# Kernel tuning notes

Hardware: AMD Instinct MI355X
Metric: run time of the kernel (lower is better)

The kernel has to match this reference:

```python
import jax, jax.numpy as jnp
import numpy as np

B, T, IN = 4096, 64, 3
D, H, NB = 128, 4, 2
DH = D // H  # 32
EPS = 1e-5


def layer_norm(x, g, b):
    mu = x.mean(-1, keepdims=True)
    v = x.var(-1, keepdims=True)
    return (x - mu) / jnp.sqrt(v + EPS) * g + b


def group_norm(x, g, b):
    # headwise GroupNorm over the last dim split into H groups of DH
    xr = x.reshape(x.shape[:-1] + (H, DH))
    mu = xr.mean(-1, keepdims=True)
    v = xr.var(-1, keepdims=True)
    xn = ((xr - mu) / jnp.sqrt(v + EPS)).reshape(x.shape)
    return xn * g + b


def slstm(xg, R):
    # xg: [B,T,4,D] input-driven gate preactivations (i,f,z,o)
    # R : [4,H,DH,DH] block-diagonal (per-head) recurrent kernels per gate
    Bb = xg.shape[0]

    def step(carry, g):
        h, c, n, m = carry  # each [B,D]
        r = jnp.einsum('bhd,ghde->bghe', h.reshape(Bb, H, DH), R).reshape(Bb, 4, D)
        g = g + r
        it, ft, zt, ot = g[:, 0], g[:, 1], g[:, 2], g[:, 3]
        m_new = jnp.maximum(ft + m, it)          # stabilizer state
        i = jnp.exp(it - m_new)                  # stabilized exp input gate
        f = jnp.exp(ft + m - m_new)              # stabilized exp forget gate
        c_new = f * c + i * jnp.tanh(zt)
        n_new = f * n + i                        # normalizer state
        h_new = jax.nn.sigmoid(ot) * c_new / n_new
        return (h_new, c_new, n_new, m_new), h_new

    init = tuple(jnp.zeros((Bb, D), xg.dtype) for _ in range(4))
    _, hs = jax.lax.scan(step, init, jnp.swapaxes(xg, 0, 1))  # [T,B,D]
    return jnp.swapaxes(hs, 0, 1)


def setup_inputs() -> dict:
    key = jax.random.key(0)
    ks = jax.random.split(key, 12)
    s_in = 1.0 / np.sqrt(IN)
    s_d = 1.0 / np.sqrt(D)
    inp = {
        'x': jax.random.normal(ks[0], (B, T, IN), jnp.float32),
        'w_in': jax.random.normal(ks[1], (IN, D), jnp.float32) * s_in,
        'b_in': jnp.zeros((D,), jnp.float32),
        'ln1_g': jnp.ones((NB, D), jnp.float32),
        'ln1_b': jnp.zeros((NB, D), jnp.float32),
        'Wg': jax.random.normal(ks[2], (NB, D, 4 * D), jnp.float32) * s_d,
        'bg': jnp.zeros((NB, 4 * D), jnp.float32),
        'Rg': jax.random.normal(ks[3], (NB, 4, H, DH, DH), jnp.float32) / np.sqrt(DH),
        'gn_g': jnp.ones((NB, D), jnp.float32),
        'gn_b': jnp.zeros((NB, D), jnp.float32),
        'ln2_g': jnp.ones((NB, D), jnp.float32),
        'ln2_b': jnp.zeros((NB, D), jnp.float32),
        'W1': jax.random.normal(ks[4], (NB, D, D), jnp.float32) * s_d,
        'W2': jax.random.normal(ks[5], (NB, D, D), jnp.float32) * s_d,
        'lnf_g': jnp.ones((D,), jnp.float32),
        'lnf_b': jnp.zeros((D,), jnp.float32),
        'w_out': jax.random.normal(ks[6], (D, 1), jnp.float32) * s_d,
        'b_out': jnp.zeros((1,), jnp.float32),
    }
    return inp


def reference(x, w_in, b_in, ln1_g, ln1_b, Wg, bg, Rg, gn_g, gn_b,
              ln2_g, ln2_b, W1, W2, lnf_g, lnf_b, w_out, b_out):
    h = x @ w_in + b_in  # [B,T,D]
    for blk in range(NB):
        # sLSTM sub-block (pre-LN residual)
        xn = layer_norm(h, ln1_g[blk], ln1_b[blk])
        xg = (xn @ Wg[blk] + bg[blk]).reshape(h.shape[0], T, 4, D)
        hs = slstm(xg, Rg[blk])
        h = h + group_norm(hs, gn_g[blk], gn_b[blk])
        # FFN sub-block (pre-LN residual, proj_factor=1.0, gelu, no bias)
        yn = layer_norm(h, ln2_g[blk], ln2_b[blk])
        h = h + jax.nn.gelu(yn @ W1[blk]) @ W2[blk]
    h = layer_norm(h, lnf_g, lnf_b)  # post-blocks norm
    out = (h[:, -1, :] @ w_out + b_out)[:, 0]  # [B]
    return out
```

## Files before the change

### kernel.cpp

```cpp
#include <hip/hip_runtime.h>
#include <hip/hip_bf16.h>
#include <cstdint>
#include <cstddef>

#define EPS 1e-5f
#define BB 4096
#define TT 64
#define NBLK 2
#define MROWS (BB * TT)

typedef unsigned short ushort_t;
typedef __attribute__((ext_vector_type(8))) short short8;
typedef __attribute__((ext_vector_type(4))) float floatx4;

__device__ __forceinline__ ushort_t f2b(float f) {
    __hip_bfloat16 h = __float2bfloat16(f);
    return *reinterpret_cast<ushort_t*>(&h);
}
__device__ __forceinline__ float tanh_fast(float z) {
    return 1.f - 2.f / (__expf(2.f * z) + 1.f);
}
__device__ __forceinline__ void lds_barrier() {
    asm volatile("s_waitcnt lgkmcnt(0)\n\ts_barrier" ::: "memory");
}

template <int CTRL>
__device__ __forceinline__ float ror_add(float v) {
    int r = __builtin_amdgcn_update_dpp(
        0, __builtin_bit_cast(int, v), CTRL, 0xf, 0xf, false);
    return v + __builtin_bit_cast(float, r);
}
__device__ __forceinline__ float red16(float v) {
    v = ror_add<0x121>(v);
    v = ror_add<0x122>(v);
    v = ror_add<0x124>(v);
    v = ror_add<0x128>(v);
    return v;
}

__global__ __launch_bounds__(256) void k_cvtall(
    const float* __restrict__ Wg, const float* __restrict__ W1,
    const float* __restrict__ W2, ushort_t* __restrict__ Wgt,
    ushort_t* __restrict__ W1t, ushort_t* __restrict__ W2t) {
    int idx = blockIdx.x * 256 + threadIdx.x;
    if (idx < 2 * 512 * 128) {
        int blk = idx >> 16, r = idx & 65535;
        int n = r >> 7, k = r & 127;
        Wgt[idx] = f2b(Wg[(size_t)blk * 65536 + k * 512 + n]);
    } else if (idx < 2 * 512 * 128 + 2 * 128 * 128) {
        int i2 = idx - 2 * 512 * 128;
        int blk = i2 >> 14, r = i2 & 16383;
        int n = r >> 7, k = r & 127;
        W1t[i2] = f2b(W1[(size_t)blk * 16384 + k * 128 + n]);
    } else {
        int i2 = idx - (2 * 512 * 128 + 2 * 128 * 128);
        int blk = i2 >> 14, r = i2 & 16383;
        int n = r >> 7, k = r & 127;
        W2t[i2] = f2b(W2[(size_t)blk * 16384 + k * 128 + n]);
    }
}

template <bool EMBED, bool LASTONLY>
__global__ __launch_bounds__(512, 2) void k_gslstm(
    float* __restrict__ h, const float* __restrict__ x,
    const float* __restrict__ w_in, const float* __restrict__ b_in,
    const ushort_t* __restrict__ Wgt, const float* __restrict__ bg,
    const float* __restrict__ Rg,
    const float* __restrict__ ln1g, const float* __restrict__ ln1b,
    const float* __restrict__ gng, const float* __restrict__ gnb) {
    __shared__ float xg_ring[2][512][20];
    __shared__ float hin_ring[3][16][132];
    __shared__ ushort_t Afrag[2][16][136];
    __shared__ ushort_t tpose[4][16][40];

    const int tid = threadIdx.x;
    const int lane = tid & 63;
    const int wave = tid >> 6;
    const int q = lane >> 4;
    const int ml = lane & 15;
    const int b0 = blockIdx.x * 16;

    if (wave < 4) {
        const int p = wave;
        const int row = p * 4 + q;
        short8 WB[4][8];
#pragma unroll
        for (int ks = 0; ks < 4; ++ks)
#pragma unroll
            for (int s = 0; s < 8; ++s)
                WB[ks][s] = *(const short8*)(Wgt +
                    ((size_t)(p * 128 + s * 16 + ml) * 128 + ks * 32 + q * 8));
        float biasv[8];
#pragma unroll
        for (int s = 0; s < 8; ++s) biasv[s] = bg[p * 128 + s * 16 + ml];

        auto issue_in = [&](int tt, float4& A, float4& B) {
            const float4* hp =
                (const float4*)(h + ((size_t)(b0 + row) * TT + tt) * 128 + ml * 8);
            A = hp[0]; B = hp[1];
        };
        auto issue_x = [&](int tt, float& x0, float& x1, float& x2) {
            const float* xp = x + ((size_t)(b0 + row) * TT + tt) * 3;
            x0 = xp[0]; x1 = xp[1]; x2 = xp[2];
        };
        auto embed_v = [&](float x0, float x1, float x2, float* v) {
            float4 w00 = *(const float4*)(w_in + 0 * 128 + ml * 8);
            float4 w01 = *(const float4*)(w_in + 0 * 128 + ml * 8 + 4);
            float4 w10 = *(const float4*)(w_in + 1 * 128 + ml * 8);
            float4 w11 = *(const float4*)(w_in + 1 * 128 + ml * 8 + 4);
            float4 w20 = *(const float4*)(w_in + 2 * 128 + ml * 8);
            float4 w21 = *(const float4*)(w_in + 2 * 128 + ml * 8 + 4);
            float4 be0 = *(const float4*)(b_in + ml * 8);
            float4 be1 = *(const float4*)(b_in + ml * 8 + 4);
            const float w0[8] = {w00.x, w00.y, w00.z, w00.w, w01.x, w01.y, w01.z, w01.w};
            const float w1[8] = {w10.x, w10.y, w10.z, w10.w, w11.x, w11.y, w11.z, w11.w};
            const float w2[8] = {w20.x, w20.y, w20.z, w20.w, w21.x, w21.y, w21.z, w21.w};
            const float be[8] = {be0.x, be0.y, be0.z, be0.w, be1.x, be1.y, be1.z, be1.w};
#pragma unroll
            for (int j = 0; j < 8; ++j)
                v[j] = x0 * w0[j] + x1 * w1[j] + x2 * w2[j] + be[j];
        };
        auto ln_stage = [&](const float* v, int aslot, int rslot) {
            float s = 0.f, ss = 0.f;
#pragma unroll
            for (int j = 0; j < 8; ++j) { s += v[j]; ss += v[j] * v[j]; }
            s = red16(s);
            ss = red16(ss);
            float mu = s * (1.f / 128.f);
            float rstd = rsqrtf(ss * (1.f / 128.f) - mu * mu + EPS);
            float4 g0 = *(const float4*)(ln1g + ml * 8);
            float4 g1 = *(const float4*)(ln1g + ml * 8 + 4);
            float4 c0 = *(const float4*)(ln1b + ml * 8);
            float4 c1 = *(const float4*)(ln1b + ml * 8 + 4);
            const float gg[8] = {g0.x, g0.y, g0.z, g0.w, g1.x, g1.y, g1.z, g1.w};
            const float bbv[8] = {c0.x, c0.y, c0.z, c0.w, c1.x, c1.y, c1.z, c1.w};
            ushort_t pk[8];
#pragma unroll
            for (int j = 0; j < 8; ++j)
                pk[j] = f2b((v[j] - mu) * rstd * gg[j] + bbv[j]);
            *(short8*)&Afrag[aslot][row][ml * 8] = *(const short8*)pk;
            *(float4*)&hin_ring[rslot][row][ml * 8] = *(const float4*)v;
            *(float4*)&hin_ring[rslot][row][ml * 8 + 4] = *(const float4*)(v + 4);
        };
        auto gemm_stage = [&](int slot) {
            short8 af[4];
#pragma unroll
            for (int ks = 0; ks < 4; ++ks)
                af[ks] = *(const short8*)&Afrag[slot][ml][ks * 32 + q * 8];
            floatx4 acc[8];
#pragma unroll
            for (int s = 0; s < 8; ++s) {
                float b = biasv[s];
                acc[s] = (floatx4){b, b, b, b};
            }
#pragma unroll
            for (int ks = 0; ks < 4; ++ks)
#pragma unroll
                for (int s = 0; s < 8; ++s)
                    acc[s] = __builtin_amdgcn_mfma_f32_16x16x32_bf16(
                        af[ks], WB[ks][s], acc[s], 0, 0, 0);
#pragma unroll
            for (int s = 0; s < 8; ++s)
                *(floatx4*)&xg_ring[slot][p * 128 + s * 16 + ml][q * 4] = acc[s];
        };

        float4 pA0, pA1, pB0, pB1;
        float px0 = 0.f, px1 = 0.f, px2 = 0.f, qx0 = 0.f, qx1 = 0.f, qx2 = 0.f;

        {
            float v[8];
            if (EMBED) {
                float a0, a1, a2, d0, d1, d2v;
                issue_x(0, a0, a1, a2);
                issue_x(1, d0, d1, d2v);
                issue_x(2, px0, px1, px2);
                embed_v(a0, a1, a2, v);  ln_stage(v, 0, 0);
                embed_v(d0, d1, d2v, v); ln_stage(v, 1, 1);
            } else {
                float4 a0, a1, d0, d1;
                issue_in(0, a0, a1);
                issue_in(1, d0, d1);
                issue_in(2, pA0, pA1);
                *(float4*)v = a0; *(float4*)(v + 4) = a1; ln_stage(v, 0, 0);
                *(float4*)v = d0; *(float4*)(v + 4) = d1; ln_stage(v, 1, 1);
            }
        }
        lds_barrier();
        gemm_stage(0);
        lds_barrier();

        int rs2 = 2, rs3 = 0;
#pragma unroll 1
        for (int t = 0; t < TT; t += 2) {
            if (t + 3 < TT) {
                if (EMBED) issue_x(t + 3, qx0, qx1, qx2);
                else       issue_in(t + 3, pB0, pB1);
            }
            gemm_stage((t + 1) & 1);
            if (t + 2 < TT) {
                float v[8];
                if (EMBED) embed_v(px0, px1, px2, v);
                else { *(float4*)v = pA0; *(float4*)(v + 4) = pA1; }
                ln_stage(v, t & 1, rs2);
            }
            lds_barrier();
            if (t + 4 < TT) {
                if (EMBED) issue_x(t + 4, px0, px1, px2);
                else       issue_in(t + 4, pA0, pA1);
            }
            if (t + 2 < TT) gemm_stage(t & 1);
            if (t + 3 < TT) {
                float v[8];
                if (EMBED) embed_v(qx0, qx1, qx2, v);
                else { *(float4*)v = pB0; *(float4*)(v + 4) = pB1; }
                ln_stage(v, (t + 1) & 1, rs3);
            }
            lds_barrier();
            rs2 += 2; if (rs2 >= 3) rs2 -= 3;
            rs3 += 2; if (rs3 >= 3) rs3 -= 3;
        }
    } else {
        __builtin_amdgcn_s_setprio(1);
        const int hd = wave - 4;
        short8 RB[4][2];
#pragma unroll
        for (int g = 0; g < 4; ++g)
#pragma unroll
            for (int d2 = 0; d2 < 2; ++d2) {
                ushort_t tmp[8];
#pragma unroll
                for (int j = 0; j < 8; ++j)
                    tmp[j] = f2b(Rg[(size_t)g * 4096 + hd * 1024 +
                                    (q * 8 + j) * 32 + d2 * 16 + ml]);
                RB[g][d2] = *(const short8*)tmp;
            }
        const float gng0 = gng[hd * 32 + ml], gng1 = gng[hd * 32 + 16 + ml];
        const float gnb0 = gnb[hd * 32 + ml], gnb1 = gnb[hd * 32 + 16 + ml];
        float cst[8], nst[8], mst[8];
#pragma unroll
        for (int i = 0; i < 8; ++i) { cst[i] = 0.f; nst[i] = 0.f; mst[i] = 0.f; }
        short8 h8 = {0, 0, 0, 0, 0, 0, 0, 0};

        auto scan_iter = [&](int t, int rs) {
            floatx4 acc[4][2];
#pragma unroll
            for (int g = 0; g < 4; ++g)
#pragma unroll
                for (int d2 = 0; d2 < 2; ++d2)
                    acc[g][d2] = *(const floatx4*)
                        &xg_ring[t & 1][g * 128 + hd * 32 + d2 * 16 + ml][q * 4];
#pragma unroll
            for (int g = 0; g < 4; ++g)
#pragma unroll
                for (int d2 = 0; d2 < 2; ++d2)
                    acc[g][d2] = __builtin_amdgcn_mfma_f32_16x16x32_bf16(
                        h8, RB[g][d2], acc[g][d2], 0, 0, 0);
            float hv[2][4];
#pragma unroll
            for (int d2 = 0; d2 < 2; ++d2)
#pragma unroll
                for (int r = 0; r < 4; ++r) {
                    const int si = d2 * 4 + r;
                    float it = acc[0][d2][r], ft = acc[1][d2][r];
                    float zt = acc[2][d2][r], ot = acc[3][d2][r];
                    float mn = fmaxf(ft + mst[si], it);
                    float iv = __expf(it - mn);
                    float fv = __expf(ft + mst[si] - mn);
                    float cn = fv * cst[si] + iv * tanh_fast(zt);
                    float nn = fv * nst[si] + iv;
                    hv[d2][r] = cn / (nn * (1.f + __expf(-ot)));
                    cst[si] = cn; nst[si] = nn; mst[si] = mn;
                }
#pragma unroll
            for (int d2 = 0; d2 < 2; ++d2)
#pragma unroll
                for (int r = 0; r < 4; ++r)
                    tpose[hd][q * 4 + r][d2 * 16 + ml] = f2b(hv[d2][r]);
            asm volatile("s_waitcnt lgkmcnt(0)" ::: "memory");
            h8 = *(const short8*)&tpose[hd][ml][q * 8];
            if (!LASTONLY || t == TT - 1) {
                float s[4], ss[4];
#pragma unroll
                for (int r = 0; r < 4; ++r) {
                    s[r] = hv[0][r] + hv[1][r];
                    ss[r] = hv[0][r] * hv[0][r] + hv[1][r] * hv[1][r];
                }
#pragma unroll
                for (int r = 0; r < 4; ++r) {
                    s[r] = red16(s[r]);
                    ss[r] = red16(ss[r]);
                }
#pragma unroll
                for (int r = 0; r < 4; ++r) {
                    float mu = s[r] * (1.f / 32.f);
                    float rstd = rsqrtf(ss[r] * (1.f / 32.f) - mu * mu + EPS);
#pragma unroll
                    for (int d2 = 0; d2 < 2; ++d2) {
                        float hin = hin_ring[rs][q * 4 + r][hd * 32 + d2 * 16 + ml];
                        float gv = d2 ? gng1 : gng0;
                        float bv = d2 ? gnb1 : gnb0;
                        h[((size_t)(b0 + q * 4 + r) * TT + t) * 128 +
                          hd * 32 + d2 * 16 + ml] =
                            hin + (hv[d2][r] - mu) * rstd * gv + bv;
                    }
                }
            }
        };

        lds_barrier();
        lds_barrier();
        int rs = 0;
#pragma unroll 1
        for (int t = 0; t < TT; t += 2) {
            scan_iter(t, rs);
            lds_barrier();
            scan_iter(t + 1, rs == 2 ? 0 : rs + 1);
            lds_barrier();
            rs += 2; if (rs >= 3) rs -= 3;
        }
    }
}

template <bool LAST>
__global__ __launch_bounds__(256, 6) void k_ffn(
    float* __restrict__ h, const ushort_t* __restrict__ W1t,
    const ushort_t* __restrict__ W2t,
    const float* __restrict__ lng, const float* __restrict__ lnb) {
    __shared__ ushort_t As[32][136];
    __shared__ ushort_t T1[32][136];
    int tid = threadIdx.x;
    int lane = tid & 63, wave = tid >> 6;
    int q = lane >> 4, ml = lane & 15;
    int wn = wave * 32;
    size_t row0 = (size_t)blockIdx.x * 32;

    short8 W1B[2][4];
#pragma unroll
    for (int jn = 0; jn < 2; ++jn)
#pragma unroll
        for (int ks = 0; ks < 4; ++ks)
            W1B[jn][ks] = *(const short8*)(W1t +
                ((size_t)(wn + jn * 16 + ml) * 128 + ks * 32 + q * 8));

    int r = tid >> 3, qd = tid & 7;
    size_t grow = LAST ? ((row0 + r) * TT + (TT - 1)) : (row0 + r);
    const float* hrow = h + grow * 128 + qd * 16;
    float s = 0.f, ss = 0.f;
#pragma unroll
    for (int k = 0; k < 4; ++k) {
        float4 v = ((const float4*)hrow)[k];
        s += v.x + v.y + v.z + v.w;
        ss += v.x * v.x + v.y * v.y + v.z * v.z + v.w * v.w;
    }
    s += __shfl_xor(s, 1); ss += __shfl_xor(ss, 1);
    s += __shfl_xor(s, 2); ss += __shfl_xor(ss, 2);
    s += __shfl_xor(s, 4); ss += __shfl_xor(ss, 4);
    float mu = s * (1.f / 128.f);
    float rstd = rsqrtf(ss * (1.f / 128.f) - mu * mu + EPS);
#pragma unroll
    for (int kk = 0; kk < 2; ++kk) {
        float4 a = ((const float4*)hrow)[2 * kk];
        float4 b = ((const float4*)hrow)[2 * kk + 1];
        int c0 = qd * 16 + kk * 8;
        float4 g0 = *(const float4*)(lng + c0);
        float4 g1 = *(const float4*)(lng + c0 + 4);
        float4 b0 = *(const float4*)(lnb + c0);
        float4 b1 = *(const float4*)(lnb + c0 + 4);
        ushort_t p[8];
        p[0] = f2b((a.x - mu) * rstd * g0.x + b0.x);
        p[1] = f2b((a.y - mu) * rstd * g0.y + b0.y);
        p[2] = f2b((a.z - mu) * rstd * g0.z + b0.z);
        p[3] = f2b((a.w - mu) * rstd * g0.w + b0.w);
        p[4] = f2b((b.x - mu) * rstd * g1.x + b1.x);
        p[5] = f2b((b.y - mu) * rstd * g1.y + b1.y);
        p[6] = f2b((b.z - mu) * rstd * g1.z + b1.z);
        p[7] = f2b((b.w - mu) * rstd * g1.w + b1.w);
        *(short8*)&As[r][c0] = *(const short8*)p;
    }
    lds_barrier();

    floatx4 acc[2][2];
#pragma unroll
    for (int i = 0; i < 2; ++i)
#pragma unroll
        for (int j = 0; j < 2; ++j) acc[i][j] = (floatx4)0.f;
#pragma unroll
    for (int ks = 0; ks < 4; ++ks) {
        short8 af[2];
#pragma unroll
        for (int im = 0; im < 2; ++im)
            af[im] = *(const short8*)&As[im * 16 + ml][ks * 32 + q * 8];
#pragma unroll
        for (int im = 0; im < 2; ++im)
#pragma unroll
            for (int jn = 0; jn < 2; ++jn)
                acc[im][jn] = __builtin_amdgcn_mfma_f32_16x16x32_bf16(
                    af[im], W1B[jn][ks], acc[im][jn], 0, 0, 0);
    }
#pragma unroll
    for (int im = 0; im < 2; ++im)
#pragma unroll
        for (int jn = 0; jn < 2; ++jn)
#pragma unroll
            for (int rr = 0; rr < 4; ++rr) {
                float v = acc[im][jn][rr];
                float u = 0.7978845608028654f * (v + 0.044715f * v * v * v);
                float gv = 0.5f * v * (1.f + tanh_fast(u));
                T1[im * 16 + q * 4 + rr][wn + jn * 16 + ml] = f2b(gv);
            }
    short8 W2B[2][4];
#pragma unroll
    for (int jn = 0; jn < 2; ++jn)
#pragma unroll
        for (int ks = 0; ks < 4; ++ks)
            W2B[jn][ks] = *(const short8*)(W2t +
                ((size_t)(wn + jn * 16 + ml) * 128 + ks * 32 + q * 8));
    lds_barrier();

#pragma unroll
    for (int i = 0; i < 2; ++i)
#pragma unroll
        for (int j = 0; j < 2; ++j) acc[i][j] = (floatx4)0.f;
#pragma unroll
    for (int ks = 0; ks < 4; ++ks) {
        short8 af[2];
#pragma unroll
        for (int im = 0; im < 2; ++im)
            af[im] = *(const short8*)&T1[im * 16 + ml][ks * 32 + q * 8];
#pragma unroll
        for (int im = 0; im < 2; ++im)
#pragma unroll
            for (int jn = 0; jn < 2; ++jn)
                acc[im][jn] = __builtin_amdgcn_mfma_f32_16x16x32_bf16(
                    af[im], W2B[jn][ks], acc[im][jn], 0, 0, 0);
    }
#pragma unroll
    for (int im = 0; im < 2; ++im)
#pragma unroll
        for (int jn = 0; jn < 2; ++jn)
#pragma unroll
            for (int rr = 0; rr < 4; ++rr) {
                int rloc = im * 16 + q * 4 + rr;
                size_t rw = LAST ? ((row0 + rloc) * TT + (TT - 1)) : (row0 + rloc);
                int cc = wn + jn * 16 + ml;
                h[rw * 128 + cc] += acc[im][jn][rr];
            }
}

__global__ __launch_bounds__(256) void k_out(const float* __restrict__ h,
                                             const float* __restrict__ lnfg,
                                             const float* __restrict__ lnfb,
                                             const float* __restrict__ w_out,
                                             const float* __restrict__ b_out,
                                             float* __restrict__ out) {
    int b = blockIdx.x * 4 + (threadIdx.x >> 6);
    int l = threadIdx.x & 63;
    const float* hr = h + ((size_t)b * TT + (TT - 1)) * 128;
    float2 v = *(const float2*)(hr + l * 2);
    float s = v.x + v.y, ss = v.x * v.x + v.y * v.y;
#pragma unroll
    for (int off = 1; off < 64; off <<= 1) {
        s += __shfl_xor(s, off);
        ss += __shfl_xor(ss, off);
    }
    float mu_ = s * (1.f / 128.f);
    float rstd = rsqrtf(ss * (1.f / 128.f) - mu_ * mu_ + EPS);
    float2 g = *(const float2*)(lnfg + l * 2);
    float2 bb = *(const float2*)(lnfb + l * 2);
    float2 w = *(const float2*)(w_out + l * 2);
    float dot = ((v.x - mu_) * rstd * g.x + bb.x) * w.x +
                ((v.y - mu_) * rstd * g.y + bb.y) * w.y;
#pragma unroll
    for (int off = 1; off < 64; off <<= 1) dot += __shfl_xor(dot, off);
    if (l == 0) out[b] = dot + b_out[0];
}

extern "C" void kernel_launch(void* const* d_in, const int* in_sizes, int n_in,
                              void* d_out, int out_size, void* d_ws, size_t ws_size,
                              hipStream_t stream) {
    const float* x    = (const float*)d_in[0];
    const float* w_in = (const float*)d_in[1];
    const float* b_in = (const float*)d_in[2];
    const float* ln1g = (const float*)d_in[3];
    const float* ln1b = (const float*)d_in[4];
    const float* Wg   = (const float*)d_in[5];
    const float* bg   = (const float*)d_in[6];
    const float* Rg   = (const float*)d_in[7];
    const float* gng  = (const float*)d_in[8];
    const float* gnb  = (const float*)d_in[9];
    const float* ln2g = (const float*)d_in[10];
    const float* ln2b = (const float*)d_in[11];
    const float* W1   = (const float*)d_in[12];
    const float* W2   = (const float*)d_in[13];
    const float* lnfg = (const float*)d_in[14];
    const float* lnfb = (const float*)d_in[15];
    const float* wout = (const float*)d_in[16];
    const float* bout = (const float*)d_in[17];
    float* out = (float*)d_out;

    float* h = (float*)d_ws;
    ushort_t* Wgt = (ushort_t*)(h + (size_t)MROWS * 128);
    ushort_t* W1t = Wgt + 2 * 512 * 128;
    ushort_t* W2t = W1t + 2 * 128 * 128;

    k_cvtall<<<(2 * 512 * 128 + 4 * 128 * 128) / 256, 256, 0, stream>>>(
        Wg, W1, W2, Wgt, W1t, W2t);

    k_gslstm<true, false><<<BB / 16, 512, 0, stream>>>(
        h, x, w_in, b_in, Wgt, bg, Rg, ln1g, ln1b, gng, gnb);
    k_ffn<false><<<MROWS / 32, 256, 0, stream>>>(h, W1t, W2t, ln2g, ln2b);
    k_gslstm<false, true><<<BB / 16, 512, 0, stream>>>(
        h, nullptr, nullptr, nullptr, Wgt + (size_t)512 * 128, bg + 512,
        Rg + (size_t)16384, ln1g + 128, ln1b + 128, gng + 128, gnb + 128);
    k_ffn<true><<<BB / 32, 256, 0, stream>>>(h, W1t + 16384, W2t + 16384,
                                             ln2g + 128, ln2b + 128);
    k_out<<<BB / 4, 256, 0, stream>>>(h, lnfg, lnfb, wout, bout, out);
}
```

Baseline: 393.1 us.

## Fuse block-0 FFN into the sLSTM kernel's GEMM waves as a pipelined per-step stage

New measurement: 514.3 us. +30.8%, slower.

```diff
diff --git a/kernel.cpp b/kernel.cpp
--- a/kernel.cpp
+++ b/kernel.cpp
@@ -22,6 +22,9 @@
 }
 __device__ __forceinline__ void lds_barrier() {
     asm volatile("s_waitcnt lgkmcnt(0)\n\ts_barrier" ::: "memory");
+}
+__device__ __forceinline__ void vm_lds_barrier() {
+    asm volatile("s_waitcnt vmcnt(0) lgkmcnt(0)\n\ts_barrier" ::: "memory");
 }
 
 template <int CTRL>
@@ -60,18 +63,22 @@
     }
 }
 
-template <bool EMBED, bool LASTONLY>
+template <bool EMBED, bool LASTONLY, bool FUSE>
 __global__ __launch_bounds__(512, 2) void k_gslstm(
     float* __restrict__ h, const float* __restrict__ x,
     const float* __restrict__ w_in, const float* __restrict__ b_in,
     const ushort_t* __restrict__ Wgt, const float* __restrict__ bg,
     const float* __restrict__ Rg,
     const float* __restrict__ ln1g, const float* __restrict__ ln1b,
-    const float* __restrict__ gng, const float* __restrict__ gnb) {
+    const float* __restrict__ gng, const float* __restrict__ gnb,
+    const ushort_t* __restrict__ W1t, const ushort_t* __restrict__ W2t,
+    const float* __restrict__ ln2g, const float* __restrict__ ln2b) {
     __shared__ float xg_ring[2][512][20];
     __shared__ float hin_ring[3][16][132];
     __shared__ ushort_t Afrag[2][16][136];
     __shared__ ushort_t tpose[4][16][40];
+    __shared__ ushort_t A2s[2][16][136];
+    __shared__ ushort_t T1s[2][16][136];
 
     const int tid = threadIdx.x;
     const int lane = tid & 63;
@@ -164,6 +171,101 @@
                 *(floatx4*)&xg_ring[slot][p * 128 + s * 16 + ml][q * 4] = acc[s];
         };
 
+        auto ffn_step = [&](int s) {
+            const int u1 = s - 1, u2 = s - 2, u3 = s - 3;
+            float4 lnA{}, lnB{};
+            if (u1 >= 0 && u1 < TT) {
+                const float4* hp = (const float4*)(h +
+                    ((size_t)(b0 + row) * TT + u1) * 128 + ml * 8);
+                lnA = hp[0]; lnB = hp[1];
+            }
+            float rres[2][4];
+            if (u3 >= 0 && u3 < TT) {
+#pragma unroll
+                for (int jn = 0; jn < 2; ++jn)
+#pragma unroll
+                    for (int rr = 0; rr < 4; ++rr)
+                        rres[jn][rr] = h[((size_t)(b0 + q * 4 + rr) * TT + u3) * 128 +
+                                         p * 32 + jn * 16 + ml];
+            }
+            if (u3 >= 0 && u3 < TT) {
+                short8 W2B[2][4];
+#pragma unroll
+                for (int jn = 0; jn < 2; ++jn)
+#pragma unroll
+                    for (int ks = 0; ks < 4; ++ks)
+                        W2B[jn][ks] = *(const short8*)(W2t +
+                            ((size_t)(p * 32 + jn * 16 + ml) * 128 + ks * 32 + q * 8));
+                short8 t1f[4];
+#pragma unroll
+                for (int ks = 0; ks < 4; ++ks)
+                    t1f[ks] = *(const short8*)&T1s[u3 & 1][ml][ks * 32 + q * 8];
+                floatx4 ac[2] = {(floatx4)0.f, (floatx4)0.f};
+#pragma unroll
+                for (int ks = 0; ks < 4; ++ks)
+#pragma unroll
+                    for (int jn = 0; jn < 2; ++jn)
+                        ac[jn] = __builtin_amdgcn_mfma_f32_16x16x32_bf16(
+                            t1f[ks], W2B[jn][ks], ac[jn], 0, 0, 0);
+#pragma unroll
+                for (int jn = 0; jn < 2; ++jn)
+#pragma unroll
+                    for (int rr = 0; rr < 4; ++rr)
+                        h[((size_t)(b0 + q * 4 + rr) * TT + u3) * 128 +
+                          p * 32 + jn * 16 + ml] = rres[jn][rr] + ac[jn][rr];
+            }
+            if (u1 >= 0 && u1 < TT) {
+                float v8[8] = {lnA.x, lnA.y, lnA.z, lnA.w, lnB.x, lnB.y, lnB.z, lnB.w};
+                float s2 = 0.f, ss2 = 0.f;
+#pragma unroll
+                for (int j = 0; j < 8; ++j) { s2 += v8[j]; ss2 += v8[j] * v8[j]; }
+                s2 = red16(s2);
+                ss2 = red16(ss2);
+                float mu = s2 * (1.f / 128.f);
+                float rstd = rsqrtf(ss2 * (1.f / 128.f) - mu * mu + EPS);
+                float4 g0 = *(const float4*)(ln2g + ml * 8);
+                float4 g1 = *(const float4*)(ln2g + ml * 8 + 4);
+                float4 c0 = *(const float4*)(ln2b + ml * 8);
+                float4 c1 = *(const float4*)(ln2b + ml * 8 + 4);
+                const float gg[8] = {g0.x, g0.y, g0.z, g0.w, g1.x, g1.y, g1.z, g1.w};
+                const float bbv[8] = {c0.x, c0.y, c0.z, c0.w, c1.x, c1.y, c1.z, c1.w};
+                ushort_t pk[8];
+#pragma unroll
+                for (int j = 0; j < 8; ++j)
+                    pk[j] = f2b((v8[j] - mu) * rstd * gg[j] + bbv[j]);
+                *(short8*)&A2s[u1 & 1][row][ml * 8] = *(const short8*)pk;
+            }
+            if (u2 >= 0 && u2 < TT) {
+                short8 W1B[2][4];
+#pragma unroll
+                for (int jn = 0; jn < 2; ++jn)
+#pragma unroll
+                    for (int ks = 0; ks < 4; ++ks)
+                        W1B[jn][ks] = *(const short8*)(W1t +
+                            ((size_t)(p * 32 + jn * 16 + ml) * 128 + ks * 32 + q * 8));
+                short8 a2f[4];
+#pragma unroll
+                for (int ks = 0; ks < 4; ++ks)
+                    a2f[ks] = *(const short8*)&A2s[u2 & 1][ml][ks * 32 + q * 8];
+                floatx4 ac[2] = {(floatx4)0.f, (floatx4)0.f};
+#pragma unroll
+                for (int ks = 0; ks < 4; ++ks)
+#pragma unroll
+                    for (int jn = 0; jn < 2; ++jn)
+                        ac[jn] = __builtin_amdgcn_mfma_f32_16x16x32_bf16(
+                            a2f[ks], W1B[jn][ks], ac[jn], 0, 0, 0);
+#pragma unroll
+                for (int jn = 0; jn < 2; ++jn)
+#pragma unroll
+                    for (int rr = 0; rr < 4; ++rr) {
+                        float v = ac[jn][rr];
+                        float u = 0.7978845608028654f * (v + 0.044715f * v * v * v);
+                        float gv = 0.5f * v * (1.f + tanh_fast(u));
+                        T1s[u2 & 1][q * 4 + rr][p * 32 + jn * 16 + ml] = f2b(gv);
+                    }
+            }
+        };
+
         float4 pA0, pA1, pB0, pB1;
         float px0 = 0.f, px1 = 0.f, px2 = 0.f, qx0 = 0.f, qx1 = 0.f, qx2 = 0.f;
 
@@ -203,6 +305,7 @@
                 else { *(float4*)v = pA0; *(float4*)(v + 4) = pA1; }
                 ln_stage(v, t & 1, rs2);
             }
+            if constexpr (FUSE) ffn_step(t);
             lds_barrier();
             if (t + 4 < TT) {
                 if (EMBED) issue_x(t + 4, px0, px1, px2);
@@ -215,9 +318,17 @@
                 else { *(float4*)v = pB0; *(float4*)(v + 4) = pB1; }
                 ln_stage(v, (t + 1) & 1, rs3);
             }
+            if constexpr (FUSE) ffn_step(t + 1);
             lds_barrier();
             rs2 += 2; if (rs2 >= 3) rs2 -= 3;
             rs3 += 2; if (rs3 >= 3) rs3 -= 3;
+        }
+        if constexpr (FUSE) {
+            ffn_step(TT);
+            lds_barrier();
+            ffn_step(TT + 1);
+            lds_barrier();
+            ffn_step(TT + 2);
         }
     } else {
         __builtin_amdgcn_s_setprio(1);
@@ -313,10 +424,14 @@
 #pragma unroll 1
         for (int t = 0; t < TT; t += 2) {
             scan_iter(t, rs);
+            if constexpr (FUSE) vm_lds_barrier(); else lds_barrier();
+            scan_iter(t + 1, rs == 2 ? 0 : rs + 1);
+            if constexpr (FUSE) vm_lds_barrier(); else lds_barrier();
+            rs += 2; if (rs >= 3) rs -= 3;
+        }
+        if constexpr (FUSE) {
             lds_barrier();
-            scan_iter(t + 1, rs == 2 ? 0 : rs + 1);
             lds_barrier();
-            rs += 2; if (rs >= 3) rs -= 3;
         }
     }
 }
@@ -506,12 +621,13 @@
     k_cvtall<<<(2 * 512 * 128 + 4 * 128 * 128) / 256, 256, 0, stream>>>(
         Wg, W1, W2, Wgt, W1t, W2t);
 
-    k_gslstm<true, false><<<BB / 16, 512, 0, stream>>>(
-        h, x, w_in, b_in, Wgt, bg, Rg, ln1g, ln1b, gng, gnb);
-    k_ffn<false><<<MROWS / 32, 256, 0, stream>>>(h, W1t, W2t, ln2g, ln2b);
-    k_gslstm<false, true><<<BB / 16, 512, 0, stream>>>(
+    k_gslstm<true, false, true><<<BB / 16, 512, 0, stream>>>(
+        h, x, w_in, b_in, Wgt, bg, Rg, ln1g, ln1b, gng, gnb,
+        W1t, W2t, ln2g, ln2b);
+    k_gslstm<false, true, false><<<BB / 16, 512, 0, stream>>>(
         h, nullptr, nullptr, nullptr, Wgt + (size_t)512 * 128, bg + 512,
-        Rg + (size_t)16384, ln1g + 128, ln1b + 128, gng + 128, gnb + 128);
+        Rg + (size_t)16384, ln1g + 128, ln1b + 128, gng + 128, gnb + 128,
+        nullptr, nullptr, nullptr, nullptr);
     k_ffn<true><<<BB / 32, 256, 0, stream>>>(h, W1t + 16384, W2t + 16384,
                                              ln2g + 128, ln2b + 128);
     k_out<<<BB / 4, 256, 0, stream>>>(h, lnfg, lnfb, wout, bout, out);
```

## Add persistent multi-tile FFN kernel with register prefetch of next row tile

Applied to the files above, without the earlier changes.

Measured after the change: 403.9 us. 1.03x slower.

```diff
diff --git a/kernel.cpp b/kernel.cpp
--- a/kernel.cpp
+++ b/kernel.cpp
@@ -166,7 +166,6 @@
 
         float4 pA0, pA1, pB0, pB1;
         float px0 = 0.f, px1 = 0.f, px2 = 0.f, qx0 = 0.f, qx1 = 0.f, qx2 = 0.f;
-
         {
             float v[8];
             if (EMBED) {
@@ -318,6 +317,161 @@
             lds_barrier();
             rs += 2; if (rs >= 3) rs -= 3;
         }
+    }
+}
+
+template <int NT>
+__global__ __launch_bounds__(256, 4) void k_ffn_pipe(
+    float* __restrict__ h, const ushort_t* __restrict__ W1t,
+    const ushort_t* __restrict__ W2t,
+    const float* __restrict__ lng, const float* __restrict__ lnb) {
+    __shared__ ushort_t As[32][136];
+    __shared__ ushort_t T1[32][136];
+    __shared__ float T2[32][132];
+    int tid = threadIdx.x;
+    int lane = tid & 63, wave = tid >> 6;
+    int q = lane >> 4, ml = lane & 15;
+    int wn = wave * 32;
+    int r = tid >> 3, qd = tid & 7;
+    size_t base = (size_t)blockIdx.x * (32 * NT);
+
+    short8 W1B[2][4];
+#pragma unroll
+    for (int jn = 0; jn < 2; ++jn)
+#pragma unroll
+        for (int ks = 0; ks < 4; ++ks)
+            W1B[jn][ks] = *(const short8*)(W1t +
+                ((size_t)(wn + jn * 16 + ml) * 128 + ks * 32 + q * 8));
+
+    float4 cur[4], nxt[4];
+    {
+        const float4* hrow = (const float4*)(h + (base + r) * 128 + qd * 16);
+#pragma unroll
+        for (int k = 0; k < 4; ++k) cur[k] = hrow[k];
+    }
+
+#pragma unroll 1
+    for (int it = 0; it < NT; ++it) {
+        if (it + 1 < NT) {
+            const float4* hrow =
+                (const float4*)(h + (base + (it + 1) * 32 + r) * 128 + qd * 16);
+#pragma unroll
+            for (int k = 0; k < 4; ++k) nxt[k] = hrow[k];
+        }
+        float s = 0.f, ss = 0.f;
+#pragma unroll
+        for (int k = 0; k < 4; ++k) {
+            float4 v = cur[k];
+            s += v.x + v.y + v.z + v.w;
+            ss += v.x * v.x + v.y * v.y + v.z * v.z + v.w * v.w;
+        }
+        s += __shfl_xor(s, 1); ss += __shfl_xor(ss, 1);
+        s += __shfl_xor(s, 2); ss += __shfl_xor(ss, 2);
+        s += __shfl_xor(s, 4); ss += __shfl_xor(ss, 4);
+        float mu = s * (1.f / 128.f);
+        float rstd = rsqrtf(ss * (1.f / 128.f) - mu * mu + EPS);
+#pragma unroll
+        for (int kk = 0; kk < 2; ++kk) {
+            float4 a = cur[2 * kk];
+            float4 b = cur[2 * kk + 1];
+            int c0 = qd * 16 + kk * 8;
+            float4 g0 = *(const float4*)(lng + c0);
+            float4 g1 = *(const float4*)(lng + c0 + 4);
+            float4 b0 = *(const float4*)(lnb + c0);
+            float4 b1 = *(const float4*)(lnb + c0 + 4);
+            ushort_t p[8];
+            p[0] = f2b((a.x - mu) * rstd * g0.x + b0.x);
+            p[1] = f2b((a.y - mu) * rstd * g0.y + b0.y);
+            p[2] = f2b((a.z - mu) * rstd * g0.z + b0.z);
+            p[3] = f2b((a.w - mu) * rstd * g0.w + b0.w);
+            p[4] = f2b((b.x - mu) * rstd * g1.x + b1.x);
+            p[5] = f2b((b.y - mu) * rstd * g1.y + b1.y);
+            p[6] = f2b((b.z - mu) * rstd * g1.z + b1.z);
+            p[7] = f2b((b.w - mu) * rstd * g1.w + b1.w);
+            *(short8*)&As[r][c0] = *(const short8*)p;
+        }
+        lds_barrier();
+
+        floatx4 acc[2][2];
+#pragma unroll
+        for (int i = 0; i < 2; ++i)
+#pragma unroll
+            for (int j = 0; j < 2; ++j) acc[i][j] = (floatx4)0.f;
+#pragma unroll
+        for (int ks = 0; ks < 4; ++ks) {
+            short8 af[2];
+#pragma unroll
+            for (int im = 0; im < 2; ++im)
+                af[im] = *(const short8*)&As[im * 16 + ml][ks * 32 + q * 8];
+#pragma unroll
+            for (int im = 0; im < 2; ++im)
+#pragma unroll
+                for (int jn = 0; jn < 2; ++jn)
+                    acc[im][jn] = __builtin_amdgcn_mfma_f32_16x16x32_bf16(
+                        af[im], W1B[jn][ks], acc[im][jn], 0, 0, 0);
+        }
+#pragma unroll
+        for (int im = 0; im < 2; ++im)
+#pragma unroll
+            for (int jn = 0; jn < 2; ++jn)
+#pragma unroll
+                for (int rr = 0; rr < 4; ++rr) {
+                    float v = acc[im][jn][rr];
+                    float u = 0.7978845608028654f * (v + 0.044715f * v * v * v);
+                    float gv = 0.5f * v * (1.f + tanh_fast(u));
+                    T1[im * 16 + q * 4 + rr][wn + jn * 16 + ml] = f2b(gv);
+                }
+        short8 W2B[2][4];
+#pragma unroll
+        for (int jn = 0; jn < 2; ++jn)
+#pragma unroll
+            for (int ks = 0; ks < 4; ++ks)
+                W2B[jn][ks] = *(const short8*)(W2t +
+                    ((size_t)(wn + jn * 16 + ml) * 128 + ks * 32 + q * 8));
+        lds_barrier();
+
+#pragma unroll
+        for (int i = 0; i < 2; ++i)
+#pragma unroll
+            for (int j = 0; j < 2; ++j) acc[i][j] = (floatx4)0.f;
+#pragma unroll
+        for (int ks = 0; ks < 4; ++ks) {
+            short8 af[2];
+#pragma unroll
+            for (int im = 0; im < 2; ++im)
+                af[im] = *(const short8*)&T1[im * 16 + ml][ks * 32 + q * 8];
+#pragma unroll
+            for (int im = 0; im < 2; ++im)
+#pragma unroll
+                for (int jn = 0; jn < 2; ++jn)
+                    acc[im][jn] = __builtin_amdgcn_mfma_f32_16x16x32_bf16(
+                        af[im], W2B[jn][ks], acc[im][jn], 0, 0, 0);
+        }
+#pragma unroll
+        for (int im = 0; im < 2; ++im)
+#pragma unroll
+            for (int jn = 0; jn < 2; ++jn)
+#pragma unroll
+                for (int rr = 0; rr < 4; ++rr)
+                    T2[im * 16 + q * 4 + rr][wn + jn * 16 + ml] = acc[im][jn][rr];
+        lds_barrier();
+
+        {
+            float* hw = h + (base + it * 32 + r) * 128 + qd * 16;
+#pragma unroll
+            for (int k = 0; k < 4; ++k) {
+                float4 t2v = *(const float4*)&T2[r][qd * 16 + k * 4];
+                float4 o;
+                o.x = cur[k].x + t2v.x;
+                o.y = cur[k].y + t2v.y;
+                o.z = cur[k].z + t2v.z;
+                o.w = cur[k].w + t2v.w;
+                ((float4*)hw)[k] = o;
+            }
+        }
+#pragma unroll
+        for (int k = 0; k < 4; ++k) cur[k] = nxt[k];
+        lds_barrier();
     }
 }
 
@@ -508,7 +662,7 @@
 
     k_gslstm<true, false><<<BB / 16, 512, 0, stream>>>(
         h, x, w_in, b_in, Wgt, bg, Rg, ln1g, ln1b, gng, gnb);
-    k_ffn<false><<<MROWS / 32, 256, 0, stream>>>(h, W1t, W2t, ln2g, ln2b);
+    k_ffn_pipe<8><<<MROWS / 256, 256, 0, stream>>>(h, W1t, W2t, ln2g, ln2b);
     k_gslstm<false, true><<<BB / 16, 512, 0, stream>>>(
         h, nullptr, nullptr, nullptr, Wgt + (size_t)512 * 128, bg + 512,
         Rg + (size_t)16384, ln1g + 128, ln1b + 128, gng + 128, gnb + 128);
```
